# Performance work log

Hardware: AMD Instinct MI355X
Metric: run time of the kernel (lower is better)

## Reference

```python
import jax, jax.numpy as jnp
import numpy as np

NUM_CLASSES = 21
THRESHOLD = 0.5
NEGPOS_RATIO = 3
VAR0, VAR1 = 0.1, 0.2


def setup_inputs() -> dict:
    B, P, T, C = 32, 32768, 64, NUM_CLASSES
    ks = jax.random.split(jax.random.key(0), 7)
    loc_pred = jax.random.normal(ks[0], (B, P, 4), jnp.float32) * 0.1
    conf_pred = jax.random.normal(ks[1], (B, P, C), jnp.float32)
    # priors in center-size form (cx, cy, w, h), all inside unit image
    cxcy = jax.random.uniform(ks[2], (P, 2), jnp.float32, 0.05, 0.95)
    wh = jax.random.uniform(ks[3], (P, 2), jnp.float32, 0.05, 0.3)
    priors = jnp.concatenate([cxcy, wh], axis=1)
    # ground-truth boxes in point form (x1, y1, x2, y2)
    xy1 = jax.random.uniform(ks[4], (B, T, 2), jnp.float32, 0.0, 0.7)
    twh = jax.random.uniform(ks[5], (B, T, 2), jnp.float32, 0.05, 0.3)
    target_boxes = jnp.concatenate([xy1, xy1 + twh], axis=2)
    labels = jax.random.randint(ks[6], (B, T), 1, C, jnp.int32)  # 0 = background
    return {"loc_pred": loc_pred, "conf_pred": conf_pred, "priors": priors,
            "target_boxes": target_boxes, "labels": labels}


def _jaccard(a, b):
    # a: [T,4] point form truths, b: [P,4] point form priors -> [T,P] IoU
    lt = jnp.maximum(a[:, None, :2], b[None, :, :2])
    rb = jnp.minimum(a[:, None, 2:], b[None, :, 2:])
    wh = jnp.clip(rb - lt, 0.0)
    inter = wh[..., 0] * wh[..., 1]
    area_a = ((a[:, 2] - a[:, 0]) * (a[:, 3] - a[:, 1]))[:, None]
    area_b = ((b[:, 2] - b[:, 0]) * (b[:, 3] - b[:, 1]))[None, :]
    return inter / (area_a + area_b - inter)


def _match(truths, labels, priors):
    # truths [T,4] point form, labels [T], priors [P,4] center-size form
    T = truths.shape[0]
    priors_pt = jnp.concatenate([priors[:, :2] - priors[:, 2:] * 0.5,
                                 priors[:, :2] + priors[:, 2:] * 0.5], axis=1)
    iou = _jaccard(truths, priors_pt)                      # [T, P]
    best_prior_idx = jnp.argmax(iou, axis=1)               # [T] best prior per truth
    best_truth_ovr = jnp.max(iou, axis=0)                  # [P]
    best_truth_idx = jnp.argmax(iou, axis=0)               # [P] best truth per prior
    # force-match: every truth keeps its best prior
    best_truth_ovr = best_truth_ovr.at[best_prior_idx].set(2.0)
    best_truth_idx = best_truth_idx.at[best_prior_idx].set(jnp.arange(T))
    matched = truths[best_truth_idx]                       # [P,4] point form
    conf = jnp.where(best_truth_ovr < THRESHOLD, 0, labels[best_truth_idx])
    # encode offsets with variances (SSD)
    g_cxcy = ((matched[:, :2] + matched[:, 2:]) * 0.5 - priors[:, :2]) / (VAR0 * priors[:, 2:])
    g_wh = jnp.log((matched[:, 2:] - matched[:, :2]) / priors[:, 2:]) / VAR1
    return jnp.concatenate([g_cxcy, g_wh], axis=1), conf


def reference(loc_pred, conf_pred, priors, target_boxes, labels):
    B, P, C = conf_pred.shape
    loc_t, conf_t = jax.vmap(lambda t, l: _match(t, l, priors))(target_boxes, labels)
    is_pos = conf_t > 0                                    # [B, P]
    # masked smooth-L1 localization loss (sum over positives)
    diff = jnp.abs(loc_pred - loc_t)
    sl1 = jnp.where(diff < 1.0, 0.5 * diff * diff, diff - 0.5)
    loss_loc = jnp.sum(sl1 * is_pos[..., None].astype(loc_pred.dtype))
    # per-prior cross entropy
    logp = jax.nn.log_softmax(conf_pred, axis=-1)
    ce = -jnp.take_along_axis(logp, conf_t[..., None], axis=-1)[..., 0]  # [B, P]
    # hard negative mining via double argsort (rank of each prior's neg loss)
    neg_conf = jnp.where(is_pos, 0.0, ce)
    loss_idx = jnp.argsort(-neg_conf, axis=1)              # descending
    idx_rank = jnp.argsort(loss_idx, axis=1)
    num_pos = jnp.sum(is_pos.astype(jnp.int32), axis=1, keepdims=True)
    num_neg = jnp.minimum(NEGPOS_RATIO * num_pos, P - 1)
    is_neg = idx_rank < num_neg
    loss_conf = jnp.sum(jnp.where(is_pos | is_neg, ce, 0.0))
    N = jnp.sum(num_pos).astype(loc_pred.dtype)
    return loss_loc / N, loss_conf / N
```

## Files before the change

### kernel.cpp

```cpp
#include <hip/hip_runtime.h>

#define NPRI 32768
#define NT 64
#define NB 32
#define NCLS 21
#define NCHUNK 32
#define NLB 64
#define TBITS 0x3F000000u

__device__ __forceinline__ float smoothl1(float d){
  float a = fabsf(d);
  return a < 1.0f ? 0.5f*a*a : a - 0.5f;
}

__global__ __launch_bounds__(256)
void k_match_ce(const float4* __restrict__ priors, const float4* __restrict__ tboxes,
                const float* __restrict__ conf, unsigned* __restrict__ bestt,
                unsigned* __restrict__ bptc, float* __restrict__ negconf){
  const int chunk = blockIdx.x, b = blockIdx.y, tid = threadIdx.x;
  __shared__ float4 tb[NT];
  __shared__ float tarea[NT];
  __shared__ unsigned tile[16][272];
  if (tid < NT){
    float4 t4 = tboxes[b*NT + tid];
    tb[tid] = t4;
    tarea[tid] = (t4.z - t4.x) * (t4.w - t4.y);
  }
  __syncthreads();
  const int p0 = chunk*1024 + tid;
  float px1_0,py1_0,px2_0,py2_0,pa_0, px1_1,py1_1,px2_1,py2_1,pa_1;
  float px1_2,py1_2,px2_2,py2_2,pa_2, px1_3,py1_3,px2_3,py2_3,pa_3;
#define SETUP(k) { float4 pr = priors[p0 + 256*k]; \
    float hx = pr.z*0.5f, hy = pr.w*0.5f; \
    px1_##k = pr.x-hx; py1_##k = pr.y-hy; px2_##k = pr.x+hx; py2_##k = pr.y+hy; \
    pa_##k = pr.z*pr.w; }
  SETUP(0) SETUP(1) SETUP(2) SETUP(3)
#undef SETUP
  const unsigned inv_0 = 1023u - (unsigned)tid;
  const unsigned inv_1 = 767u  - (unsigned)tid;
  const unsigned inv_2 = 511u  - (unsigned)tid;
  const unsigned inv_3 = 255u  - (unsigned)tid;
  unsigned bp_0 = 0u, bp_1 = 0u, bp_2 = 0u, bp_3 = 0u;

  const int pc = chunk*1024 + tid*4;
  const float4* g4 = (const float4*)(conf + ((size_t)b*NPRI + pc)*NCLS);
  float s0=0.f,s1=0.f,s2=0.f,s3=0.f, x00=0.f,x01=0.f,x02=0.f,x03=0.f;
  float4 cb0,cb1,cb2,cb3,cb4,cb5;
#define CELL(idx, f) { float e = __expf(f); \
    if ((idx) < 21)      { s0 += e; if ((idx) == 0)  x00 = f; } \
    else if ((idx) < 42) { s1 += e; if ((idx) == 21) x01 = f; } \
    else if ((idx) < 63) { s2 += e; if ((idx) == 42) x02 = f; } \
    else                 { s3 += e; if ((idx) == 63) x03 = f; } }
#define CONS(j, B) CELL(4*(j)+0, B.x) CELL(4*(j)+1, B.y) CELL(4*(j)+2, B.z) CELL(4*(j)+3, B.w)

#define GROUP(g) { \
    _Pragma("unroll 4") \
    for (int t16 = 0; t16 < 16; ++t16){ \
      const int t = (g)*16 + t16; \
      const float4 t4 = tb[t]; \
      const float ta = tarea[t]; \
      unsigned q0, q1, q2, q3; \
      IOU(0) IOU(1) IOU(2) IOU(3) \
      unsigned m01 = q0 > q1 ? q0 : q1; \
      unsigned m23 = q2 > q3 ? q2 : q3; \
      tile[t16][tid] = m01 > m23 ? m01 : m23; \
    } \
    __syncthreads(); \
    { \
      const int r = tid >> 4, j = tid & 15; \
      unsigned mx = 0u; \
      _Pragma("unroll") \
      for (int i = 0; i < 16; ++i){ \
        unsigned v = tile[r][i*16 + j]; \
        mx = mx > v ? mx : v; \
      } \
      _Pragma("unroll") \
      for (int off = 1; off < 16; off <<= 1){ \
        unsigned o = (unsigned)__shfl_xor((int)mx, off); \
        mx = mx > o ? mx : o; \
      } \
      if (j == 0) \
        bptc[((size_t)b*NT + (g)*16 + r)*NCHUNK + chunk] = mx; \
    } \
    __syncthreads(); }
#define IOU(k) { \
    float w = fminf(t4.z,px2_##k) - fmaxf(t4.x,px1_##k); \
    float h = fminf(t4.w,py2_##k) - fmaxf(t4.y,py1_##k); \
    w = fmaxf(w,0.f); h = fmaxf(h,0.f); \
    float inter = w*h; \
    float iou = inter * __builtin_amdgcn_rcpf(ta + pa_##k - inter); \
    unsigned ib = __float_as_uint(iou); \
    unsigned pk = (ib & 0xFFFFFFC0u) | (unsigned)(63 - t); \
    if (pk > bp_##k) bp_##k = pk; \
    q##k = (ib & 0xFFFFFC00u) | inv_##k; }

  cb0 = g4[0]; cb1 = g4[1]; cb2 = g4[2]; cb3 = g4[3]; cb4 = g4[4];
  GROUP(0)
  CONS(0,cb0) CONS(1,cb1) CONS(2,cb2) CONS(3,cb3) CONS(4,cb4)
  cb0 = g4[5]; cb1 = g4[6]; cb2 = g4[7]; cb3 = g4[8]; cb4 = g4[9];
  GROUP(1)
  CONS(5,cb0) CONS(6,cb1) CONS(7,cb2) CONS(8,cb3) CONS(9,cb4)
  cb0 = g4[10]; cb1 = g4[11]; cb2 = g4[12]; cb3 = g4[13]; cb4 = g4[14];
  GROUP(2)
  CONS(10,cb0) CONS(11,cb1) CONS(12,cb2) CONS(13,cb3) CONS(14,cb4)
  cb0 = g4[15]; cb1 = g4[16]; cb2 = g4[17]; cb3 = g4[18]; cb4 = g4[19]; cb5 = g4[20];
  GROUP(3)
  CONS(15,cb0) CONS(16,cb1) CONS(17,cb2) CONS(18,cb3) CONS(19,cb4) CONS(20,cb5)
#undef IOU
#undef GROUP
#undef CONS
#undef CELL

  const size_t ob = (size_t)b*NPRI + p0;
  bestt[ob]       = bp_0;
  bestt[ob + 256] = bp_1;
  bestt[ob + 512] = bp_2;
  bestt[ob + 768] = bp_3;
  float4 o;
  o.x = __logf(s0) - x00;
  o.y = __logf(s1) - x01;
  o.z = __logf(s2) - x02;
  o.w = __logf(s3) - x03;
  *(float4*)(negconf + (size_t)b*NPRI + pc) = o;
}

__global__ __launch_bounds__(256)
void k_loss(const float4* __restrict__ priors, const float4* __restrict__ tboxes,
            const int* __restrict__ labels, const float* __restrict__ conf,
            const float4* __restrict__ loc, const unsigned* __restrict__ bestt,
            const unsigned* __restrict__ bptc, float* __restrict__ negconf,
            float* __restrict__ part_loc, float* __restrict__ part_ce,
            int* __restrict__ part_cnt){
  const int b = blockIdx.y, tid = threadIdx.x;
  const int base = blockIdx.x * 512;
  __shared__ float4 tb[NT];
  __shared__ int slab[NT];
  __shared__ int fm[512];
  fm[tid] = -1; fm[tid + 256] = -1;
  if (tid < NT){
    tb[tid] = tboxes[b*NT + tid];
    slab[tid] = labels[b*NT + tid];
  }
  __syncthreads();
  if (tid < NT){
    const unsigned* src = bptc + ((size_t)b*NT + tid)*NCHUNK;
    unsigned kk = 0u; int bc = 0;
    #pragma unroll
    for (int c = 0; c < NCHUNK; ++c){
      unsigned v = src[c];
      if (v > kk){ kk = v; bc = c; }
    }
    const int p = bc*1024 + 1023 - (int)(kk & 1023u);
    unsigned d = (unsigned)(p - base);
    if (d < 512u) atomicMax(&fm[d], tid);
  }
  __syncthreads();
  float lloc = 0.f, posce = 0.f;
  int cnt = 0;
  #pragma unroll
  for (int k = 0; k < 2; ++k){
    const int sl = tid + 256*k;
    const int p = base + sl;
    const size_t idx = (size_t)b*NPRI + p;
    const unsigned bt = bestt[idx];
    const int f = fm[sl];
    if ((f >= 0) || (bt >= TBITS)){
      const int t = (f >= 0) ? f : (63 - (int)(bt & 63u));
      float4 pr = priors[p];
      float4 t4 = tb[t];
      float4 lp = loc[idx];
      float gcx = ((t4.x+t4.z)*0.5f - pr.x) / (0.1f*pr.z);
      float gcy = ((t4.y+t4.w)*0.5f - pr.y) / (0.1f*pr.w);
      float gw = __logf((t4.z-t4.x)/pr.z) * 5.f;
      float gh = __logf((t4.w-t4.y)/pr.w) * 5.f;
      lloc += smoothl1(lp.x-gcx)+smoothl1(lp.y-gcy)+smoothl1(lp.z-gw)+smoothl1(lp.w-gh);
      const int cls = slab[t];
      posce += negconf[idx] + conf[idx*NCLS] - conf[idx*NCLS + cls];
      negconf[idx] = 0.f;
      cnt++;
    }
  }
  for (int off = 32; off; off >>= 1){
    lloc  += __shfl_xor(lloc, off);
    posce += __shfl_xor(posce, off);
    cnt   += __shfl_xor(cnt, off);
  }
  __shared__ float r0[4], r1[4];
  __shared__ int r2[4];
  if ((tid & 63) == 0){ int w = tid>>6; r0[w]=lloc; r1[w]=posce; r2[w]=cnt; }
  __syncthreads();
  if (tid == 0){
    float a0=0.f, a1=0.f; int c=0;
    #pragma unroll
    for (int w = 0; w < 4; ++w){ a0+=r0[w]; a1+=r1[w]; c+=r2[w]; }
    const int o = b*NLB + blockIdx.x;
    part_loc[o] = a0;
    part_ce[o]  = a1;
    part_cnt[o] = c;
  }
}

__global__ __launch_bounds__(1024)
void k_mine(const float* __restrict__ negconf, const int* __restrict__ part_cnt,
            float* __restrict__ part_mine){
  const int b = blockIdx.x, tid = threadIdx.x;
  __shared__ int sk;
  if (tid < NLB){
    int c = part_cnt[b*NLB + tid];
    for (int off = 32; off; off >>= 1) c += __shfl_xor(c, off);
    if (tid == 0) sk = min(3*c, NPRI-1);
  }
  __syncthreads();
  const int k = sk;
  if (k <= 0){ if (tid == 0) part_mine[b] = 0.f; return; }
  const float* nc = negconf + (size_t)b*NPRI;
  unsigned v[32];
  #pragma unroll
  for (int i = 0; i < 32; ++i) v[i] = __float_as_uint(nc[tid + i*1024]);
  __shared__ int scnt[2][16];
  unsigned cur = 0u;
  for (int bit = 30; bit >= 0; --bit){
    const unsigned cand = cur | (1u << bit);
    int c = 0;
    #pragma unroll
    for (int i = 0; i < 32; ++i)
      c += (int)__popcll(__ballot(v[i] >= cand));
    if ((tid & 63) == 0) scnt[bit & 1][tid>>6] = c;
    __syncthreads();
    int tot = 0;
    #pragma unroll
    for (int w = 0; w < 16; ++w) tot += scnt[bit & 1][w];
    if (tot >= k) cur = cand;
  }
  float sgt = 0.f; int cgt = 0;
  #pragma unroll
  for (int i = 0; i < 32; ++i){
    if (v[i] > cur){ sgt += __uint_as_float(v[i]); cgt++; }
  }
  for (int off = 32; off; off >>= 1){
    sgt += __shfl_xor(sgt, off);
    cgt += __shfl_xor(cgt, off);
  }
  __shared__ float ss[16];
  __shared__ int sc[16];
  if ((tid & 63) == 0){ ss[tid>>6] = sgt; sc[tid>>6] = cgt; }
  __syncthreads();
  if (tid == 0){
    float st = 0.f; int ct = 0;
    #pragma unroll
    for (int w = 0; w < 16; ++w){ st += ss[w]; ct += sc[w]; }
    part_mine[b] = st + (float)(k - ct) * __uint_as_float(cur);
  }
}

__global__ __launch_bounds__(1024)
void k_final(const float* __restrict__ part_loc, const float* __restrict__ part_ce,
             const int* __restrict__ part_cnt, const float* __restrict__ part_mine,
             float* __restrict__ out){
  const int tid = threadIdx.x;
  float sl = 0.f, se = 0.f; int sc_ = 0;
  #pragma unroll
  for (int i = tid; i < NB*NLB; i += 1024){
    sl += part_loc[i];
    se += part_ce[i];
    sc_ += part_cnt[i];
  }
  float sm = (tid < NB) ? part_mine[tid] : 0.f;
  for (int off = 32; off; off >>= 1){
    sl += __shfl_xor(sl, off);
    se += __shfl_xor(se, off);
    sm += __shfl_xor(sm, off);
    sc_ += __shfl_xor(sc_, off);
  }
  __shared__ float a0[16], a1[16], a2[16];
  __shared__ int a3[16];
  if ((tid & 63) == 0){ int w = tid>>6; a0[w]=sl; a1[w]=se; a2[w]=sm; a3[w]=sc_; }
  __syncthreads();
  if (tid == 0){
    float t0=0.f, t1=0.f, t2=0.f; int n=0;
    #pragma unroll
    for (int w = 0; w < 16; ++w){ t0+=a0[w]; t1+=a1[w]; t2+=a2[w]; n+=a3[w]; }
    float N = (float)n;
    out[0] = t0 / N;
    out[1] = (t1 + t2) / N;
  }
}

extern "C" void kernel_launch(void* const* d_in, const int* in_sizes, int n_in,
                              void* d_out, int out_size, void* d_ws, size_t ws_size,
                              hipStream_t stream){
  (void)in_sizes; (void)n_in; (void)out_size; (void)ws_size;
  const float4* loc    = (const float4*)d_in[0];
  const float*  conf   = (const float*) d_in[1];
  const float4* priors = (const float4*)d_in[2];
  const float4* tboxes = (const float4*)d_in[3];
  const int*    labels = (const int*)   d_in[4];
  float* out = (float*)d_out;

  char* ws = (char*)d_ws;
  size_t off = 0;
  float* negconf = (float*)(ws + off);            off += (size_t)NB*NPRI*4;
  unsigned* bestt = (unsigned*)(ws + off);        off += (size_t)NB*NPRI*4;
  unsigned* bptc = (unsigned*)(ws + off);         off += (size_t)NB*NT*NCHUNK*4;
  float* part_loc = (float*)(ws + off);           off += (size_t)NB*NLB*4;
  float* part_ce  = (float*)(ws + off);           off += (size_t)NB*NLB*4;
  int*   part_cnt = (int*)(ws + off);             off += (size_t)NB*NLB*4;
  float* part_mine = (float*)(ws + off);          off += NB*4;

  k_match_ce<<<dim3(NCHUNK, NB), 256, 0, stream>>>(priors, tboxes, conf,
                                                   bestt, bptc, negconf);
  k_loss <<<dim3(NLB, NB), 256, 0, stream>>>(priors, tboxes, labels, conf, loc,
                                             bestt, bptc, negconf,
                                             part_loc, part_ce, part_cnt);
  k_mine <<<NB, 1024, 0, stream>>>(negconf, part_cnt, part_mine);
  k_final<<<1, 1024, 0, stream>>>(part_loc, part_ce, part_cnt, part_mine, out);
}
```

Measured before the change: 86.33 us.

## Fuse per-prior loss and hard-negative mining into one per-batch kernel

Merges the positive-loss kernel and the radix-select mining kernel into a single 1024-thread block per batch image. Negative confidences are held in registers and positives are masked there, so negconf is no longer written back to global memory and one launch is dropped. Force-matched priors are tracked with a shared bitmask and handled separately by the first 64 threads, and the final reduction becomes a single-thread loop over 32 partials. The cost is lower parallelism for the loss part: 32 blocks instead of 2048.

```diff
diff --git a/kernel.cpp b/kernel.cpp
--- a/kernel.cpp
+++ b/kernel.cpp
@@ -5,7 +5,6 @@
 #define NB 32
 #define NCLS 21
 #define NCHUNK 32
-#define NLB 64
 #define TBITS 0x3F000000u
 
 __device__ __forceinline__ float smoothl1(float d){
@@ -124,25 +123,22 @@
   *(float4*)(negconf + (size_t)b*NPRI + pc) = o;
 }
 
-__global__ __launch_bounds__(256)
-void k_loss(const float4* __restrict__ priors, const float4* __restrict__ tboxes,
-            const int* __restrict__ labels, const float* __restrict__ conf,
-            const float4* __restrict__ loc, const unsigned* __restrict__ bestt,
-            const unsigned* __restrict__ bptc, float* __restrict__ negconf,
-            float* __restrict__ part_loc, float* __restrict__ part_ce,
-            int* __restrict__ part_cnt){
-  const int b = blockIdx.y, tid = threadIdx.x;
-  const int base = blockIdx.x * 512;
+__global__ __launch_bounds__(1024)
+void k_lossmine(const float4* __restrict__ priors, const float4* __restrict__ tboxes,
+                const int* __restrict__ labels, const float* __restrict__ conf,
+                const float4* __restrict__ loc, const unsigned* __restrict__ bestt,
+                const unsigned* __restrict__ bptc, const float* __restrict__ negconf,
+                float* __restrict__ part_loc, float* __restrict__ part_ce,
+                int* __restrict__ part_cnt, float* __restrict__ part_mine){
+  const int b = blockIdx.x, tid = threadIdx.x;
   __shared__ float4 tb[NT];
   __shared__ int slab[NT];
-  __shared__ int fm[512];
-  fm[tid] = -1; fm[tid + 256] = -1;
+  __shared__ int sbpi[NT];
+  __shared__ unsigned fmw[1024];
+  fmw[tid] = 0u;
   if (tid < NT){
     tb[tid] = tboxes[b*NT + tid];
     slab[tid] = labels[b*NT + tid];
-  }
-  __syncthreads();
-  if (tid < NT){
     const unsigned* src = bptc + ((size_t)b*NT + tid)*NCHUNK;
     unsigned kk = 0u; int bc = 0;
     #pragma unroll
@@ -150,22 +146,29 @@
       unsigned v = src[c];
       if (v > kk){ kk = v; bc = c; }
     }
-    const int p = bc*1024 + 1023 - (int)(kk & 1023u);
-    unsigned d = (unsigned)(p - base);
-    if (d < 512u) atomicMax(&fm[d], tid);
-  }
-  __syncthreads();
+    sbpi[tid] = bc*1024 + 1023 - (int)(kk & 1023u);
+  }
+  __syncthreads();
+  if (tid < NT){
+    const int p = sbpi[tid];
+    atomicOr(&fmw[p >> 5], 1u << (p & 31));
+  }
+  __syncthreads();
+
   float lloc = 0.f, posce = 0.f;
   int cnt = 0;
+  unsigned v[32];
+  const size_t bb = (size_t)b*NPRI;
   #pragma unroll
-  for (int k = 0; k < 2; ++k){
-    const int sl = tid + 256*k;
-    const int p = base + sl;
-    const size_t idx = (size_t)b*NPRI + p;
+  for (int i = 0; i < 32; ++i){
+    const int p = tid + i*1024;
+    const size_t idx = bb + p;
     const unsigned bt = bestt[idx];
-    const int f = fm[sl];
-    if ((f >= 0) || (bt >= TBITS)){
-      const int t = (f >= 0) ? f : (63 - (int)(bt & 63u));
+    const float nc = negconf[idx];
+    const bool forced = (fmw[(tid >> 5) + i*32] >> (tid & 31)) & 1u;
+    const bool posn = (bt >= TBITS) && !forced;
+    if (posn){
+      const int t = 63 - (int)(bt & 63u);
       float4 pr = priors[p];
       float4 t4 = tb[t];
       float4 lp = loc[idx];
@@ -175,8 +178,28 @@
       float gh = __logf((t4.w-t4.y)/pr.w) * 5.f;
       lloc += smoothl1(lp.x-gcx)+smoothl1(lp.y-gcy)+smoothl1(lp.z-gw)+smoothl1(lp.w-gh);
       const int cls = slab[t];
+      posce += nc + conf[idx*NCLS] - conf[idx*NCLS + cls];
+      cnt++;
+    }
+    v[i] = (forced || bt >= TBITS) ? 0u : __float_as_uint(nc);
+  }
+  if (tid < NT){
+    const int p = sbpi[tid];
+    bool keep = true;
+    for (int t2 = tid + 1; t2 < NT; ++t2)
+      if (sbpi[t2] == p) keep = false;
+    if (keep){
+      const size_t idx = bb + p;
+      float4 pr = priors[p];
+      float4 t4 = tb[tid];
+      float4 lp = loc[idx];
+      float gcx = ((t4.x+t4.z)*0.5f - pr.x) / (0.1f*pr.z);
+      float gcy = ((t4.y+t4.w)*0.5f - pr.y) / (0.1f*pr.w);
+      float gw = __logf((t4.z-t4.x)/pr.z) * 5.f;
+      float gh = __logf((t4.w-t4.y)/pr.w) * 5.f;
+      lloc += smoothl1(lp.x-gcx)+smoothl1(lp.y-gcy)+smoothl1(lp.z-gw)+smoothl1(lp.w-gh);
+      const int cls = slab[tid];
       posce += negconf[idx] + conf[idx*NCLS] - conf[idx*NCLS + cls];
-      negconf[idx] = 0.f;
       cnt++;
     }
   }
@@ -185,38 +208,23 @@
     posce += __shfl_xor(posce, off);
     cnt   += __shfl_xor(cnt, off);
   }
-  __shared__ float r0[4], r1[4];
-  __shared__ int r2[4];
+  __shared__ float r0[16], r1[16];
+  __shared__ int r2[16];
   if ((tid & 63) == 0){ int w = tid>>6; r0[w]=lloc; r1[w]=posce; r2[w]=cnt; }
   __syncthreads();
+  __shared__ int snp;
   if (tid == 0){
     float a0=0.f, a1=0.f; int c=0;
     #pragma unroll
-    for (int w = 0; w < 4; ++w){ a0+=r0[w]; a1+=r1[w]; c+=r2[w]; }
-    const int o = b*NLB + blockIdx.x;
-    part_loc[o] = a0;
-    part_ce[o]  = a1;
-    part_cnt[o] = c;
-  }
-}
-
-__global__ __launch_bounds__(1024)
-void k_mine(const float* __restrict__ negconf, const int* __restrict__ part_cnt,
-            float* __restrict__ part_mine){
-  const int b = blockIdx.x, tid = threadIdx.x;
-  __shared__ int sk;
-  if (tid < NLB){
-    int c = part_cnt[b*NLB + tid];
-    for (int off = 32; off; off >>= 1) c += __shfl_xor(c, off);
-    if (tid == 0) sk = min(3*c, NPRI-1);
-  }
-  __syncthreads();
-  const int k = sk;
+    for (int w = 0; w < 16; ++w){ a0+=r0[w]; a1+=r1[w]; c+=r2[w]; }
+    part_loc[b] = a0;
+    part_ce[b]  = a1;
+    part_cnt[b] = c;
+    snp = c;
+  }
+  __syncthreads();
+  const int k = min(3*snp, NPRI-1);
   if (k <= 0){ if (tid == 0) part_mine[b] = 0.f; return; }
-  const float* nc = negconf + (size_t)b*NPRI;
-  unsigned v[32];
-  #pragma unroll
-  for (int i = 0; i < 32; ++i) v[i] = __float_as_uint(nc[tid + i*1024]);
   __shared__ int scnt[2][16];
   unsigned cur = 0u;
   for (int bit = 30; bit >= 0; --bit){
@@ -253,36 +261,20 @@
   }
 }
 
-__global__ __launch_bounds__(1024)
+__global__ __launch_bounds__(64)
 void k_final(const float* __restrict__ part_loc, const float* __restrict__ part_ce,
              const int* __restrict__ part_cnt, const float* __restrict__ part_mine,
              float* __restrict__ out){
-  const int tid = threadIdx.x;
-  float sl = 0.f, se = 0.f; int sc_ = 0;
-  #pragma unroll
-  for (int i = tid; i < NB*NLB; i += 1024){
-    sl += part_loc[i];
-    se += part_ce[i];
-    sc_ += part_cnt[i];
-  }
-  float sm = (tid < NB) ? part_mine[tid] : 0.f;
-  for (int off = 32; off; off >>= 1){
-    sl += __shfl_xor(sl, off);
-    se += __shfl_xor(se, off);
-    sm += __shfl_xor(sm, off);
-    sc_ += __shfl_xor(sc_, off);
-  }
-  __shared__ float a0[16], a1[16], a2[16];
-  __shared__ int a3[16];
-  if ((tid & 63) == 0){ int w = tid>>6; a0[w]=sl; a1[w]=se; a2[w]=sm; a3[w]=sc_; }
-  __syncthreads();
-  if (tid == 0){
-    float t0=0.f, t1=0.f, t2=0.f; int n=0;
-    #pragma unroll
-    for (int w = 0; w < 16; ++w){ t0+=a0[w]; t1+=a1[w]; t2+=a2[w]; n+=a3[w]; }
+  if (threadIdx.x == 0){
+    float t0 = 0.f, t1 = 0.f; int n = 0;
+    for (int b = 0; b < NB; ++b){
+      t0 += part_loc[b];
+      t1 += part_ce[b] + part_mine[b];
+      n  += part_cnt[b];
+    }
     float N = (float)n;
     out[0] = t0 / N;
-    out[1] = (t1 + t2) / N;
+    out[1] = t1 / N;
   }
 }
 
@@ -302,16 +294,15 @@
   float* negconf = (float*)(ws + off);            off += (size_t)NB*NPRI*4;
   unsigned* bestt = (unsigned*)(ws + off);        off += (size_t)NB*NPRI*4;
   unsigned* bptc = (unsigned*)(ws + off);         off += (size_t)NB*NT*NCHUNK*4;
-  float* part_loc = (float*)(ws + off);           off += (size_t)NB*NLB*4;
-  float* part_ce  = (float*)(ws + off);           off += (size_t)NB*NLB*4;
-  int*   part_cnt = (int*)(ws + off);             off += (size_t)NB*NLB*4;
+  float* part_loc = (float*)(ws + off);           off += (size_t)NB*4;
+  float* part_ce  = (float*)(ws + off);           off += (size_t)NB*4;
+  int*   part_cnt = (int*)(ws + off);             off += (size_t)NB*4;
   float* part_mine = (float*)(ws + off);          off += NB*4;
 
   k_match_ce<<<dim3(NCHUNK, NB), 256, 0, stream>>>(priors, tboxes, conf,
                                                    bestt, bptc, negconf);
-  k_loss <<<dim3(NLB, NB), 256, 0, stream>>>(priors, tboxes, labels, conf, loc,
-                                             bestt, bptc, negconf,
-                                             part_loc, part_ce, part_cnt);
-  k_mine <<<NB, 1024, 0, stream>>>(negconf, part_cnt, part_mine);
-  k_final<<<1, 1024, 0, stream>>>(part_loc, part_ce, part_cnt, part_mine, out);
-}
+  k_lossmine<<<NB, 1024, 0, stream>>>(priors, tboxes, labels, conf, loc,
+                                      bestt, bptc, negconf,
+                                      part_loc, part_ce, part_cnt, part_mine);
+  k_final<<<1, 64, 0, stream>>>(part_loc, part_ce, part_cnt, part_mine, out);
+}
```

Measured after the change: 108.6 us. 1.26x slower.
